# Kernel optimization log

Measured on AMD Instinct MI355X. Metric: run time of the kernel, lower is better.

## Reference

```python
import jax, jax.numpy as jnp
import numpy as np

B, S, D, H, DQ, DV = 4, 2048, 1024, 16, 64, 64

def setup_inputs() -> dict:
    key = jax.random.key(0)
    ks = jax.random.split(key, 11)
    s_in = 1.0 / np.sqrt(D)
    s_o = 1.0 / np.sqrt(H * DV)
    return {
        "query": jax.random.normal(ks[0], (B, S, D), jnp.float32),
        "key":   jax.random.normal(ks[1], (B, S, D), jnp.float32),
        "value": jax.random.normal(ks[2], (B, S, D), jnp.float32),
        "Wq_w": jax.random.normal(ks[3], (D, H * DQ), jnp.float32) * s_in,
        "Wq_b": jax.random.normal(ks[4], (H * DQ,), jnp.float32) * s_in,
        "Wk_w": jax.random.normal(ks[5], (D, H * DQ), jnp.float32) * s_in,
        "Wk_b": jax.random.normal(ks[6], (H * DQ,), jnp.float32) * s_in,
        "Wv_w": jax.random.normal(ks[7], (D, H * DV), jnp.float32) * s_in,
        "Wv_b": jax.random.normal(ks[8], (H * DV,), jnp.float32) * s_in,
        "Wo_w": jax.random.normal(ks[9], (H * DV, D), jnp.float32) * s_o,
        "Wo_b": jax.random.normal(ks[10], (D,), jnp.float32) * s_o,
    }

def reference(query, key, value, Wq_w, Wq_b, Wk_w, Wk_b, Wv_w, Wv_b, Wo_w, Wo_b):
    b, s, d = query.shape
    # chunk(h, dim=-1) + cat(dim=0) == split last dim into (h, dq) per-head slices
    q = (query @ Wq_w + Wq_b).reshape(b, s, H, DQ)  # bshq
    k = (key   @ Wk_w + Wk_b).reshape(b, s, H, DQ)
    v = (value @ Wv_w + Wv_b).reshape(b, s, H, DV)
    # NOTE: source scales by sqrt(K) where K = seq_len (query.shape[1])
    scores = jnp.einsum("bshq,bthq->bhst", q, k) / jnp.sqrt(jnp.float32(s))
    attn = jax.nn.softmax(scores, axis=-1)          # (b, h, s, s)
    out = jnp.einsum("bhst,bthv->bshv", attn, v).reshape(b, s, H * DV)
    return out @ Wo_w + Wo_b
```

## Files before the change

### kernel.cpp

```cpp
#include <hip/hip_runtime.h>
#include <hip/hip_bf16.h>
#include <cstdint>


typedef __attribute__((ext_vector_type(4))) float f32x4;
typedef __attribute__((ext_vector_type(8))) short bf16x8;

#define GLB const __attribute__((address_space(1))) void*
#define LDS __attribute__((address_space(3))) void*

__device__ __forceinline__ ushort f2bf(float f) {
    uint32_t u = __builtin_bit_cast(uint32_t, f);
    u += 0x7fffu + ((u >> 16) & 1u);
    return (ushort)(u >> 16);
}

__device__ __forceinline__ uint32_t cvt_pk_bf16(float lo, float hi) {
    uint32_t r;
    asm("v_cvt_pk_bf16_f32 %0, %1, %2" : "=v"(r) : "v"(lo), "v"(hi));
    return r;
}

__global__ void convert3(const float* __restrict__ a, const float* __restrict__ b,
                         const float* __restrict__ c,
                         ushort* __restrict__ oa, ushort* __restrict__ ob,
                         ushort* __restrict__ oc, int n4) {
    const float* in = blockIdx.y == 0 ? a : blockIdx.y == 1 ? b : c;
    ushort* out     = blockIdx.y == 0 ? oa : blockIdx.y == 1 ? ob : oc;
    for (int i = blockIdx.x * blockDim.x + threadIdx.x; i < n4; i += gridDim.x * blockDim.x) {
        float4 v = reinterpret_cast<const float4*>(in)[i];
        ushort4 o;
        o.x = f2bf(v.x); o.y = f2bf(v.y); o.z = f2bf(v.z); o.w = f2bf(v.w);
        reinterpret_cast<ushort4*>(out)[i] = o;
    }
}

__global__ void transpose_w4(const float* __restrict__ w0, const float* __restrict__ w1,
                             const float* __restrict__ w2, const float* __restrict__ w3,
                             ushort* __restrict__ o0, ushort* __restrict__ o1,
                             ushort* __restrict__ o2, ushort* __restrict__ o3) {
    const float* in = blockIdx.z == 0 ? w0 : blockIdx.z == 1 ? w1 : blockIdx.z == 2 ? w2 : w3;
    ushort* out     = blockIdx.z == 0 ? o0 : blockIdx.z == 1 ? o1 : blockIdx.z == 2 ? o2 : o3;
    __shared__ float tile[64][65];
    const int tx = threadIdx.x & 63, ty = threadIdx.x >> 6;
    const int nb = blockIdx.x * 64, kb = blockIdx.y * 64;
#pragma unroll
    for (int i = ty; i < 64; i += 4)
        tile[i][tx] = in[(size_t)(kb + i) * 1024 + nb + tx];
    __syncthreads();
#pragma unroll
    for (int i = ty; i < 64; i += 4)
        out[(size_t)(nb + i) * 1024 + kb + tx] = f2bf(tile[tx][i]);
}

#define GEMM_BODY(A_, BT_)                                                          \
    f32x4 acc[4][4] = {};                                                           \
    for (int k0 = 0; k0 < 1024; k0 += 64) {                                         \
        _Pragma("unroll")                                                           \
        for (int p = 0; p < 4; ++p) {                                               \
            const int gr = (p * 256 + tid) >> 3;                                    \
            const int sc = ((tid & 7) * 16) ^ ((gr & 7) << 4);                      \
            const int lo = (p * 256 + (tid & ~63)) * 8;                             \
            __builtin_amdgcn_global_load_lds((GLB)(A_  + (size_t)(mb + gr) * 1024 + k0 + (sc >> 1)), (LDS)(As + lo), 16, 0, 0); \
            __builtin_amdgcn_global_load_lds((GLB)(BT_ + (size_t)(nb + gr) * 1024 + k0 + (sc >> 1)), (LDS)(Bs + lo), 16, 0, 0); \
        }                                                                           \
        __syncthreads();                                                            \
        _Pragma("unroll")                                                           \
        for (int kc = 0; kc < 2; ++kc) {                                            \
            bf16x8 af[4], bfr[4];                                                   \
            _Pragma("unroll")                                                       \
            for (int i = 0; i < 4; ++i) {                                           \
                const int ar = wr * 64 + i * 16 + r;                                \
                const int br = wc * 64 + i * 16 + r;                                \
                af[i]  = *(const bf16x8*)((const char*)As + ar * 128 + ((kc * 64 + g * 16) ^ ((ar & 7) << 4))); \
                bfr[i] = *(const bf16x8*)((const char*)Bs + br * 128 + ((kc * 64 + g * 16) ^ ((br & 7) << 4))); \
            }                                                                       \
            __builtin_amdgcn_s_setprio(1);                                          \
            _Pragma("unroll")                                                       \
            for (int mi = 0; mi < 4; ++mi)                                          \
                _Pragma("unroll")                                                   \
                for (int ni = 0; ni < 4; ++ni)                                      \
                    acc[mi][ni] = __builtin_amdgcn_mfma_f32_16x16x32_bf16(af[mi], bfr[ni], acc[mi][ni], 0, 0, 0); \
            __builtin_amdgcn_s_setprio(0);                                          \
        }                                                                           \
        __syncthreads();                                                            \
    }

__global__ __launch_bounds__(256) void gemm_qkv(const ushort* __restrict__ qb,
                                                const ushort* __restrict__ kb,
                                                const ushort* __restrict__ vb,
                                                const ushort* __restrict__ WqT,
                                                const ushort* __restrict__ WkT,
                                                const ushort* __restrict__ WvT,
                                                const float* __restrict__ Wq_b,
                                                const float* __restrict__ Wk_b,
                                                const float* __restrict__ Wv_b,
                                                ushort* __restrict__ Qp,
                                                ushort* __restrict__ Kp,
                                                ushort* __restrict__ Vt,
                                                float qscale) {
    __shared__ ushort As[128 * 64];
    __shared__ ushort Bs[128 * 64];
    const int tid = threadIdx.x;
    const int lane = tid & 63;
    const int wave = tid >> 6, wr = wave >> 1, wc = wave & 1;
    const int r = lane & 15, g = lane >> 4;
    const int proj = blockIdx.y;
    const int id = blockIdx.x;
    const int xcd = id & 7, j = id >> 3;
    const int bx = j >> 3, by = xcd * 8 + (j & 7);
    const int mb = by * 128, nb = bx * 128;

    const ushort* A    = proj == 0 ? qb : proj == 1 ? kb : vb;
    const ushort* BT   = proj == 0 ? WqT : proj == 1 ? WkT : WvT;
    const float*  bias = proj == 0 ? Wq_b : proj == 1 ? Wk_b : Wv_b;

    GEMM_BODY(A, BT)

    const float oscale = proj == 0 ? qscale : 1.0f;
#pragma unroll
    for (int ni = 0; ni < 4; ++ni) {
        const int col = nb + wc * 64 + ni * 16 + r;
        const float bv = bias[col];
#pragma unroll
        for (int mi = 0; mi < 4; ++mi) {
            const int m0 = mb + wr * 64 + mi * 16 + g * 4;
            if (proj < 2) {
                ushort* C = proj == 0 ? Qp : Kp;
#pragma unroll
                for (int i = 0; i < 4; ++i)
                    C[(size_t)(m0 + i) * 1024 + col] = f2bf((acc[mi][ni][i] + bv) * oscale);
            } else {
                const int b = m0 >> 11, s = m0 & 2047;
                const int h = col >> 6, dv = col & 63;
                ushort4 o;
                o.x = f2bf(acc[mi][ni][0] + bv);
                o.y = f2bf(acc[mi][ni][1] + bv);
                o.z = f2bf(acc[mi][ni][2] + bv);
                o.w = f2bf(acc[mi][ni][3] + bv);
                *(ushort4*)&Vt[(((size_t)(b * 16 + h) * 64 + dv) << 11) + s] = o;
            }
        }
    }
}

__global__ __launch_bounds__(256) void gemm_out(const ushort* __restrict__ A_,
                                                const ushort* __restrict__ BT_,
                                                const float* __restrict__ bias,
                                                float* __restrict__ Cf) {
    __shared__ ushort As[128 * 64];
    __shared__ ushort Bs[128 * 64];
    const int tid = threadIdx.x;
    const int lane = tid & 63;
    const int wave = tid >> 6, wr = wave >> 1, wc = wave & 1;
    const int r = lane & 15, g = lane >> 4;
    const int id = blockIdx.x;
    const int xcd = id & 7, j = id >> 3;
    const int bx = j >> 3, by = xcd * 8 + (j & 7);
    const int mb = by * 128, nb = bx * 128;

    GEMM_BODY(A_, BT_)

#pragma unroll
    for (int ni = 0; ni < 4; ++ni) {
        const int col = nb + wc * 64 + ni * 16 + r;
        const float bv = bias[col];
#pragma unroll
        for (int mi = 0; mi < 4; ++mi) {
            const int m0 = mb + wr * 64 + mi * 16 + g * 4;
#pragma unroll
            for (int i = 0; i < 4; ++i)
                Cf[(size_t)(m0 + i) * 1024 + col] = acc[mi][ni][i] + bv;
        }
    }
}

__global__ __launch_bounds__(512, 4) void attn_kernel(const ushort* __restrict__ Qp,
                                                      const ushort* __restrict__ Kp,
                                                      const ushort* __restrict__ Vt,
                                                      ushort* __restrict__ AO) {
    const int tid = threadIdx.x;
    const int lane = tid & 63, wave = tid >> 6;
    const int r = lane & 15, g = lane >> 4;
    const int id = blockIdx.x;
    const int xcd = id & 7, j = id >> 3;
    const int qt = j & 7;
    const int grp = xcd * 8 + (j >> 3);
    const int h = grp & 15, b = grp >> 4;
    const int qbase = qt * 256 + wave * 32;

    const ushort* Qh = Qp + (size_t)b * 2048 * 1024 + h * 64;
    const ushort* Kh = Kp + (size_t)b * 2048 * 1024 + h * 64;
    const ushort* Vh = Vt + ((size_t)(b * 16 + h)) * 64 * 2048;

    __shared__ ushort Ks[2][64 * 64];
    __shared__ ushort Vs[2][64 * 64];
    __shared__ ushort Pl[8][32 * 64];
    ushort* Pw = (ushort*)Pl[wave];

    const int srow = tid >> 3;
    const int scb  = ((tid & 7) * 16) ^ ((srow & 7) << 4);
    const int wlds = wave * 512;
    const ushort* gKn = Kh + (size_t)srow * 1024 + (scb >> 1) + 64 * 1024;
    const ushort* gVn = Vh + (size_t)srow * 2048 + (scb >> 1) + 64;

    int fro[4][2];
#pragma unroll
    for (int tf = 0; tf < 4; ++tf)
#pragma unroll
        for (int kc = 0; kc < 2; ++kc) {
            const int row = tf * 16 + r;
            fro[tf][kc] = row * 128 + ((kc * 64 + g * 16) ^ ((row & 7) << 4));
        }
    int pwo[2][4], pro[2][2];
#pragma unroll
    for (int gg = 0; gg < 2; ++gg) {
        const int row = gg * 16 + r;
#pragma unroll
        for (int tf = 0; tf < 4; ++tf)
            pwo[gg][tf] = row * 128 + ((tf * 32 + g * 8) ^ ((row & 7) << 4));
#pragma unroll
        for (int kc = 0; kc < 2; ++kc)
            pro[gg][kc] = row * 128 + ((kc * 64 + g * 16) ^ ((row & 7) << 4));
    }

    bf16x8 qf[2][2];
#pragma unroll
    for (int gg = 0; gg < 2; ++gg)
#pragma unroll
        for (int kc = 0; kc < 2; ++kc)
            qf[gg][kc] = *(const bf16x8*)&Qh[(size_t)(qbase + gg * 16 + r) * 1024 + kc * 32 + g * 8];

    f32x4 oacc[2][4] = {};
    float ell[2] = {0.f, 0.f};

    __builtin_amdgcn_global_load_lds((GLB)(gKn - 64 * 1024), (LDS)(Ks[0] + wlds), 16, 0, 0);
    __builtin_amdgcn_global_load_lds((GLB)(gVn - 64), (LDS)(Vs[0] + wlds), 16, 0, 0);
    __syncthreads();

    for (int t0 = 0; t0 < 2048; t0 += 64) {
        const int cur = (t0 >> 6) & 1;
        if (t0 + 64 < 2048) {
            __builtin_amdgcn_global_load_lds((GLB)gKn, (LDS)(Ks[cur ^ 1] + wlds), 16, 0, 0);
            __builtin_amdgcn_global_load_lds((GLB)gVn, (LDS)(Vs[cur ^ 1] + wlds), 16, 0, 0);
            gKn += 64 * 1024;
            gVn += 64;
        }

        const char* Kb = (const char*)Ks[cur];
        bf16x8 kf[4][2];
#pragma unroll
        for (int tf = 0; tf < 4; ++tf)
#pragma unroll
            for (int kc = 0; kc < 2; ++kc)
                kf[tf][kc] = *(const bf16x8*)(Kb + fro[tf][kc]);

        f32x4 st[2][4] = {};
        __builtin_amdgcn_s_setprio(1);
#pragma unroll
        for (int gg = 0; gg < 2; ++gg)
#pragma unroll
            for (int tf = 0; tf < 4; ++tf)
#pragma unroll
                for (int kc = 0; kc < 2; ++kc)
                    st[gg][tf] = __builtin_amdgcn_mfma_f32_16x16x32_bf16(kf[tf][kc], qf[gg][kc], st[gg][tf], 0, 0, 0);
        __builtin_amdgcn_s_setprio(0);

#pragma unroll
        for (int gg = 0; gg < 2; ++gg) {
            float psum = 0.f;
#pragma unroll
            for (int tf = 0; tf < 4; ++tf) {
                const float p0 = __builtin_amdgcn_exp2f(st[gg][tf][0]);
                const float p1 = __builtin_amdgcn_exp2f(st[gg][tf][1]);
                const float p2 = __builtin_amdgcn_exp2f(st[gg][tf][2]);
                const float p3 = __builtin_amdgcn_exp2f(st[gg][tf][3]);
                psum += (p0 + p1) + (p2 + p3);
                uint2 pk;
                pk.x = cvt_pk_bf16(p0, p1);
                pk.y = cvt_pk_bf16(p2, p3);
                *(uint2*)((char*)Pw + pwo[gg][tf]) = pk;
            }
            psum += __shfl_xor(psum, 16);
            psum += __shfl_xor(psum, 32);
            ell[gg] += psum;
        }

        const char* Vb = (const char*)Vs[cur];
        bf16x8 vf[4][2];
#pragma unroll
        for (int mf = 0; mf < 4; ++mf)
#pragma unroll
            for (int kc = 0; kc < 2; ++kc)
                vf[mf][kc] = *(const bf16x8*)(Vb + fro[mf][kc]);

        __builtin_amdgcn_s_setprio(1);
#pragma unroll
        for (int gg = 0; gg < 2; ++gg) {
#pragma unroll
            for (int kc = 0; kc < 2; ++kc) {
                const bf16x8 pf = *(const bf16x8*)((const char*)Pw + pro[gg][kc]);
#pragma unroll
                for (int mf = 0; mf < 4; ++mf)
                    oacc[gg][mf] = __builtin_amdgcn_mfma_f32_16x16x32_bf16(vf[mf][kc], pf, oacc[gg][mf], 0, 0, 0);
            }
        }
        __builtin_amdgcn_s_setprio(0);

        __syncthreads();
    }

#pragma unroll
    for (int gg = 0; gg < 2; ++gg) {
        const float inv = 1.f / ell[gg];
        const int q = qbase + gg * 16 + r;
#pragma unroll
        for (int mf = 0; mf < 4; ++mf) {
            ushort4 o;
            o.x = f2bf(oacc[gg][mf][0] * inv);
            o.y = f2bf(oacc[gg][mf][1] * inv);
            o.z = f2bf(oacc[gg][mf][2] * inv);
            o.w = f2bf(oacc[gg][mf][3] * inv);
            *(ushort4*)&AO[(size_t)(b * 2048 + q) * 1024 + h * 64 + mf * 16 + g * 4] = o;
        }
    }
}

extern "C" void kernel_launch(void* const* d_in, const int* in_sizes, int n_in,
                              void* d_out, int out_size, void* d_ws, size_t ws_size,
                              hipStream_t stream) {
    const float* q_f  = (const float*)d_in[0];
    const float* k_f  = (const float*)d_in[1];
    const float* v_f  = (const float*)d_in[2];
    const float* Wq_w = (const float*)d_in[3];
    const float* Wq_b = (const float*)d_in[4];
    const float* Wk_w = (const float*)d_in[5];
    const float* Wk_b = (const float*)d_in[6];
    const float* Wv_w = (const float*)d_in[7];
    const float* Wv_b = (const float*)d_in[8];
    const float* Wo_w = (const float*)d_in[9];
    const float* Wo_b = (const float*)d_in[10];
    float* out = (float*)d_out;
    char* ws = (char*)d_ws;

    const size_t MB = 1ull << 20;
    ushort* qb  = (ushort*)(ws);
    ushort* kb  = (ushort*)(ws + 16 * MB);
    ushort* vb  = (ushort*)(ws + 32 * MB);
    ushort* WqT = (ushort*)(ws + 48 * MB);
    ushort* WkT = (ushort*)(ws + 50 * MB);
    ushort* WvT = (ushort*)(ws + 52 * MB);
    ushort* WoT = (ushort*)(ws + 54 * MB);
    ushort* Qp  = (ushort*)(ws + 56 * MB);
    ushort* Kp  = (ushort*)(ws + 72 * MB);
    ushort* Vt  = (ushort*)(ws + 88 * MB);
    ushort* AO  = qb;

    const int n4 = (4 * 2048 * 1024) / 4;
    convert3<<<dim3(1024, 3), 256, 0, stream>>>(q_f, k_f, v_f, qb, kb, vb, n4);

    transpose_w4<<<dim3(16, 16, 4), 256, 0, stream>>>(Wq_w, Wk_w, Wv_w, Wo_w,
                                                      WqT, WkT, WvT, WoT);

    constexpr float QSCALE = (float)(1.4426950408889634 / 45.254833995939045);

    gemm_qkv<<<dim3(512, 3), 256, 0, stream>>>(qb, kb, vb, WqT, WkT, WvT,
                                               Wq_b, Wk_b, Wv_b, Qp, Kp, Vt, QSCALE);

    attn_kernel<<<512, 512, 0, stream>>>(Qp, Kp, Vt, AO);

    gemm_out<<<512, 256, 0, stream>>>(AO, WoT, Wo_b, out);
}
```

Measured before the change: 208.6 us.

## Double-buffer GEMM K-loop and merge input conversion with weight transpose

The GEMM main loop now uses a K-step of 32 with two LDS buffers, so the load of the next tile is issued before computing on the current one. It drops the XOR swizzle, which may bring back LDS bank conflicts. The separate input-conversion and weight-transpose kernels are merged into one launch, and the conversion now uses packed bf16 converts on 8 elements per thread. The goal is to hide global-load latency and cut launch overhead. In exchange there are twice as many barriers per K element, with less work per barrier.

Measured after the change: 204.2 us. 1.02x faster.

```diff
diff --git a/kernel.cpp b/kernel.cpp
--- a/kernel.cpp
+++ b/kernel.cpp
@@ -21,68 +21,77 @@
     return r;
 }
 
-__global__ void convert3(const float* __restrict__ a, const float* __restrict__ b,
-                         const float* __restrict__ c,
-                         ushort* __restrict__ oa, ushort* __restrict__ ob,
-                         ushort* __restrict__ oc, int n4) {
-    const float* in = blockIdx.y == 0 ? a : blockIdx.y == 1 ? b : c;
-    ushort* out     = blockIdx.y == 0 ? oa : blockIdx.y == 1 ? ob : oc;
-    for (int i = blockIdx.x * blockDim.x + threadIdx.x; i < n4; i += gridDim.x * blockDim.x) {
-        float4 v = reinterpret_cast<const float4*>(in)[i];
-        ushort4 o;
-        o.x = f2bf(v.x); o.y = f2bf(v.y); o.z = f2bf(v.z); o.w = f2bf(v.w);
-        reinterpret_cast<ushort4*>(out)[i] = o;
-    }
-}
-
-__global__ void transpose_w4(const float* __restrict__ w0, const float* __restrict__ w1,
-                             const float* __restrict__ w2, const float* __restrict__ w3,
-                             ushort* __restrict__ o0, ushort* __restrict__ o1,
-                             ushort* __restrict__ o2, ushort* __restrict__ o3) {
-    const float* in = blockIdx.z == 0 ? w0 : blockIdx.z == 1 ? w1 : blockIdx.z == 2 ? w2 : w3;
-    ushort* out     = blockIdx.z == 0 ? o0 : blockIdx.z == 1 ? o1 : blockIdx.z == 2 ? o2 : o3;
+__global__ void prep(const float* __restrict__ qf, const float* __restrict__ kf,
+                     const float* __restrict__ vf,
+                     const float* __restrict__ w0, const float* __restrict__ w1,
+                     const float* __restrict__ w2, const float* __restrict__ w3,
+                     ushort* __restrict__ oq, ushort* __restrict__ ok,
+                     ushort* __restrict__ ov,
+                     ushort* __restrict__ t0, ushort* __restrict__ t1,
+                     ushort* __restrict__ t2, ushort* __restrict__ t3, int n8) {
     __shared__ float tile[64][65];
-    const int tx = threadIdx.x & 63, ty = threadIdx.x >> 6;
-    const int nb = blockIdx.x * 64, kb = blockIdx.y * 64;
-#pragma unroll
-    for (int i = ty; i < 64; i += 4)
-        tile[i][tx] = in[(size_t)(kb + i) * 1024 + nb + tx];
-    __syncthreads();
-#pragma unroll
-    for (int i = ty; i < 64; i += 4)
-        out[(size_t)(nb + i) * 1024 + kb + tx] = f2bf(tile[tx][i]);
-}
+    const int y = blockIdx.y;
+    if (y < 3) {
+        const float* in = y == 0 ? qf : y == 1 ? kf : vf;
+        ushort* out     = y == 0 ? oq : y == 1 ? ok : ov;
+        for (int i = blockIdx.x * blockDim.x + threadIdx.x; i < n8; i += gridDim.x * blockDim.x) {
+            const float4 a = reinterpret_cast<const float4*>(in)[2 * i];
+            const float4 b = reinterpret_cast<const float4*>(in)[2 * i + 1];
+            uint4 o;
+            o.x = cvt_pk_bf16(a.x, a.y);
+            o.y = cvt_pk_bf16(a.z, a.w);
+            o.z = cvt_pk_bf16(b.x, b.y);
+            o.w = cvt_pk_bf16(b.z, b.w);
+            reinterpret_cast<uint4*>(out)[i] = o;
+        }
+    } else {
+        const int x = blockIdx.x;
+        const int wz = x >> 8, wy = (x >> 4) & 15, wx = x & 15;
+        const float* in = wz == 0 ? w0 : wz == 1 ? w1 : wz == 2 ? w2 : w3;
+        ushort* out     = wz == 0 ? t0 : wz == 1 ? t1 : wz == 2 ? t2 : t3;
+        const int tx = threadIdx.x & 63, ty = threadIdx.x >> 6;
+        const int nb = wx * 64, kb = wy * 64;
+#pragma unroll
+        for (int i = ty; i < 64; i += 4)
+            tile[i][tx] = in[(size_t)(kb + i) * 1024 + nb + tx];
+        __syncthreads();
+#pragma unroll
+        for (int i = ty; i < 64; i += 4)
+            out[(size_t)(nb + i) * 1024 + kb + tx] = f2bf(tile[tx][i]);
+    }
+}
+
+#define GEMM_STAGE(A_, BT_, k0, Ad, Bd)                                             \
+    _Pragma("unroll")                                                               \
+    for (int jj = 0; jj < 2; ++jj) {                                                \
+        const int t = jj * 256 + tid;                                               \
+        const int lo = (jj * 256 + (tid & ~63)) * 8;                                \
+        __builtin_amdgcn_global_load_lds((GLB)(A_  + (size_t)(mb + (t >> 2)) * 1024 + (k0) + (t & 3) * 8), (LDS)(Ad + lo), 16, 0, 0); \
+        __builtin_amdgcn_global_load_lds((GLB)(BT_ + (size_t)(nb + (t >> 2)) * 1024 + (k0) + (t & 3) * 8), (LDS)(Bd + lo), 16, 0, 0); \
+    }
 
 #define GEMM_BODY(A_, BT_)                                                          \
     f32x4 acc[4][4] = {};                                                           \
-    for (int k0 = 0; k0 < 1024; k0 += 64) {                                         \
+    GEMM_STAGE(A_, BT_, 0, As[0], Bs[0])                                            \
+    __syncthreads();                                                                \
+    for (int k0 = 0; k0 < 1024; k0 += 32) {                                         \
+        const int cur = (k0 >> 5) & 1;                                              \
+        if (k0 + 32 < 1024) {                                                       \
+            GEMM_STAGE(A_, BT_, k0 + 32, As[cur ^ 1], Bs[cur ^ 1])                  \
+        }                                                                           \
+        bf16x8 af[4], bfr[4];                                                       \
         _Pragma("unroll")                                                           \
-        for (int p = 0; p < 4; ++p) {                                               \
-            const int gr = (p * 256 + tid) >> 3;                                    \
-            const int sc = ((tid & 7) * 16) ^ ((gr & 7) << 4);                      \
-            const int lo = (p * 256 + (tid & ~63)) * 8;                             \
-            __builtin_amdgcn_global_load_lds((GLB)(A_  + (size_t)(mb + gr) * 1024 + k0 + (sc >> 1)), (LDS)(As + lo), 16, 0, 0); \
-            __builtin_amdgcn_global_load_lds((GLB)(BT_ + (size_t)(nb + gr) * 1024 + k0 + (sc >> 1)), (LDS)(Bs + lo), 16, 0, 0); \
+        for (int i = 0; i < 4; ++i) {                                               \
+            af[i]  = *(const bf16x8*)&As[cur][(wr * 64 + i * 16 + r) * 32 + g * 8]; \
+            bfr[i] = *(const bf16x8*)&Bs[cur][(wc * 64 + i * 16 + r) * 32 + g * 8]; \
         }                                                                           \
-        __syncthreads();                                                            \
+        __builtin_amdgcn_s_setprio(1);                                              \
         _Pragma("unroll")                                                           \
-        for (int kc = 0; kc < 2; ++kc) {                                            \
-            bf16x8 af[4], bfr[4];                                                   \
+        for (int mi = 0; mi < 4; ++mi)                                              \
             _Pragma("unroll")                                                       \
-            for (int i = 0; i < 4; ++i) {                                           \
-                const int ar = wr * 64 + i * 16 + r;                                \
-                const int br = wc * 64 + i * 16 + r;                                \
-                af[i]  = *(const bf16x8*)((const char*)As + ar * 128 + ((kc * 64 + g * 16) ^ ((ar & 7) << 4))); \
-                bfr[i] = *(const bf16x8*)((const char*)Bs + br * 128 + ((kc * 64 + g * 16) ^ ((br & 7) << 4))); \
-            }                                                                       \
-            __builtin_amdgcn_s_setprio(1);                                          \
-            _Pragma("unroll")                                                       \
-            for (int mi = 0; mi < 4; ++mi)                                          \
-                _Pragma("unroll")                                                   \
-                for (int ni = 0; ni < 4; ++ni)                                      \
-                    acc[mi][ni] = __builtin_amdgcn_mfma_f32_16x16x32_bf16(af[mi], bfr[ni], acc[mi][ni], 0, 0, 0); \
-            __builtin_amdgcn_s_setprio(0);                                          \
-        }                                                                           \
+            for (int ni = 0; ni < 4; ++ni)                                          \
+                acc[mi][ni] = __builtin_amdgcn_mfma_f32_16x16x32_bf16(af[mi], bfr[ni], acc[mi][ni], 0, 0, 0); \
+        __builtin_amdgcn_s_setprio(0);                                              \
         __syncthreads();                                                            \
     }
 
@@ -99,8 +108,8 @@
                                                 ushort* __restrict__ Kp,
                                                 ushort* __restrict__ Vt,
                                                 float qscale) {
-    __shared__ ushort As[128 * 64];
-    __shared__ ushort Bs[128 * 64];
+    __shared__ ushort As[2][128 * 32];
+    __shared__ ushort Bs[2][128 * 32];
     const int tid = threadIdx.x;
     const int lane = tid & 63;
     const int wave = tid >> 6, wr = wave >> 1, wc = wave & 1;
@@ -148,8 +157,8 @@
                                                 const ushort* __restrict__ BT_,
                                                 const float* __restrict__ bias,
                                                 float* __restrict__ Cf) {
-    __shared__ ushort As[128 * 64];
-    __shared__ ushort Bs[128 * 64];
+    __shared__ ushort As[2][128 * 32];
+    __shared__ ushort Bs[2][128 * 32];
     const int tid = threadIdx.x;
     const int lane = tid & 63;
     const int wave = tid >> 6, wr = wave >> 1, wc = wave & 1;
@@ -356,11 +365,9 @@
     ushort* Vt  = (ushort*)(ws + 88 * MB);
     ushort* AO  = qb;
 
-    const int n4 = (4 * 2048 * 1024) / 4;
-    convert3<<<dim3(1024, 3), 256, 0, stream>>>(q_f, k_f, v_f, qb, kb, vb, n4);
-
-    transpose_w4<<<dim3(16, 16, 4), 256, 0, stream>>>(Wq_w, Wk_w, Wv_w, Wo_w,
-                                                      WqT, WkT, WvT, WoT);
+    const int n8 = (4 * 2048 * 1024) / 8;
+    prep<<<dim3(1024, 4), 256, 0, stream>>>(q_f, k_f, v_f, Wq_w, Wk_w, Wv_w, Wo_w,
+                                            qb, kb, vb, WqT, WkT, WvT, WoT, n8);
 
     constexpr float QSCALE = (float)(1.4426950408889634 / 45.254833995939045);
 
```
